# Kernel optimization log

Hardware: AMD Instinct MI355X
Metric: run time of the kernel (lower is better)

The kernel has to match this reference:

```python
import jax, jax.numpy as jnp
import numpy as np

B, S, D, H = 2, 2048, 1024, 16
DH = D // H


def setup_inputs() -> dict:
    key = jax.random.key(0)
    ks = jax.random.split(key, 13)
    s = 1.0 / np.sqrt(D)
    inp = {
        "q": jax.random.normal(ks[0], (B, S, D), jnp.float32),
        "k": jax.random.normal(ks[1], (B, S, D), jnp.float32),
        "v": jax.random.normal(ks[2], (B, S, D), jnp.float32),
        # causal mask [B,1,Q,K]: True = attend
        "attn_mask": jnp.broadcast_to(jnp.tril(jnp.ones((S, S), bool))[None, None], (B, 1, S, S)),
        "rel_bias": 0.1 * jax.random.normal(ks[3], (H, S, S), jnp.float32),
        "Wq": s * jax.random.normal(ks[4], (D, D), jnp.float32),
        "bq": jnp.zeros((D,), jnp.float32),
        "Wk": s * jax.random.normal(ks[5], (D, D), jnp.float32),
        "bk": jnp.zeros((D,), jnp.float32),
        "Wv": s * jax.random.normal(ks[6], (D, D), jnp.float32),
        "bv": jnp.zeros((D,), jnp.float32),
        "Wo": s * jax.random.normal(ks[7], (D, D), jnp.float32),
        "bo": jnp.zeros((D,), jnp.float32),
    }
    return inp


def reference(q, k, v, attn_mask, rel_bias, Wq, bq, Wk, bk, Wv, bv, Wo, bo):
    Bq, Q, Dm = q.shape
    K = k.shape[1]
    # projections -> [B, H, S, DH]
    qh = (q @ Wq + bq).reshape(Bq, Q, H, DH).transpose(0, 2, 1, 3)
    kh = (k @ Wk + bk).reshape(Bq, K, H, DH).transpose(0, 2, 1, 3)
    vh = (v @ Wv + bv).reshape(Bq, K, H, DH).transpose(0, 2, 1, 3)
    scores = jnp.einsum("bhqd,bhkd->bhqk", qh, kh) / np.sqrt(DH).astype(np.float32)
    scores = scores + rel_bias  # [H,Q,K] broadcasts over batch
    scores = jnp.where(attn_mask, scores, -jnp.inf)
    attn = jax.nn.softmax(scores, axis=-1)
    out = jnp.einsum("bhqk,bhkd->bhqd", attn, vh)
    out = out.transpose(0, 2, 1, 3).reshape(Bq, Q, Dm)
    return out @ Wo + bo
```

## Files before the change

### kernel.cpp

```cpp
#include <hip/hip_runtime.h>

typedef unsigned short u16;
typedef __attribute__((ext_vector_type(8))) short bf16x8;
typedef __attribute__((ext_vector_type(4))) float f32x4;
typedef __attribute__((ext_vector_type(4))) unsigned short us4;

#define B_ 2
#define S_ 2048
#define D_ 1024
#define H_ 16
#define DH_ 64
#define M_ 4096

__device__ __forceinline__ u16 f2bf(float f) {
  unsigned int u = __builtin_bit_cast(unsigned int, f);
  u += 0x7FFFu + ((u >> 16) & 1u);
  return (u16)(u >> 16);
}

__device__ __forceinline__ unsigned int cvtpk(float lo, float hi) {
  unsigned int r;
  asm("v_cvt_pk_bf16_f32 %0, %1, %2" : "=v"(r) : "v"(lo), "v"(hi));
  return r;
}

__device__ __forceinline__ float fexp2(float x) {
  float r;
  asm("v_exp_f32 %0, %1" : "=v"(r) : "v"(x));
  return r;
}

__device__ __forceinline__ void gload_lds16(const void* g, void* l) {
  __builtin_amdgcn_global_load_lds(
      (__attribute__((address_space(1))) void*)(g),
      (__attribute__((address_space(3))) void*)(l),
      16, 0, 0);
}

__global__ __launch_bounds__(256) void wprep_kernel(const float* __restrict__ W0,
                                                    const float* __restrict__ W1,
                                                    const float* __restrict__ W2,
                                                    const float* __restrict__ W3,
                                                    u16* __restrict__ Wt,
                                                    const float* __restrict__ qin,
                                                    const float* __restrict__ kin,
                                                    const float* __restrict__ vin,
                                                    u16* __restrict__ Xq,
                                                    u16* __restrict__ Xk,
                                                    u16* __restrict__ Xv) {
  int z = blockIdx.z;
  if (z < 4) {
    __shared__ float tile[32][33];
    const float* W = (z == 0) ? W0 : (z == 1) ? W1 : (z == 2) ? W2 : W3;
    u16* out = Wt + (size_t)z * D_ * D_;
    int tx = threadIdx.x, ty = threadIdx.y;
    int x = blockIdx.x * 32 + tx;
    for (int j = 0; j < 32; j += 8)
      tile[ty + j][tx] = W[(size_t)(blockIdx.y * 32 + ty + j) * D_ + x];
    __syncthreads();
    int x2 = blockIdx.y * 32 + tx;
    for (int j = 0; j < 32; j += 8)
      out[(size_t)(blockIdx.x * 32 + ty + j) * D_ + x2] = f2bf(tile[tx][ty + j]);
  } else {
    int zz = z - 4;
    const float* src = (zz == 0) ? qin : (zz == 1) ? kin : vin;
    u16* dst = (zz == 0) ? Xq : (zz == 1) ? Xk : Xv;
    int bid = blockIdx.y * 32 + blockIdx.x;
    int t = threadIdx.y * 32 + threadIdx.x;
    const float4* s4 = (const float4*)src;
    for (int i = 0; i < 4; ++i) {
      int idx = bid * 1024 + i * 256 + t;
      float4 v4 = s4[idx];
      us4 o;
      o[0] = f2bf(v4.x); o[1] = f2bf(v4.y); o[2] = f2bf(v4.z); o[3] = f2bf(v4.w);
      ((us4*)dst)[idx] = o;
    }
  }
}

__global__ __launch_bounds__(256) void gemm_qkv(const u16* __restrict__ Xq,
                                                const u16* __restrict__ Xk,
                                                const u16* __restrict__ Xv,
                                                const u16* __restrict__ Wt,
                                                const float* __restrict__ bq,
                                                const float* __restrict__ bk,
                                                const float* __restrict__ bv,
                                                u16* __restrict__ Qh,
                                                u16* __restrict__ Kh,
                                                u16* __restrict__ Vt) {
  __shared__ u16 As[128 * 32];
  __shared__ u16 Bs[128 * 32];
  int fid = blockIdx.x;
  int xcd = fid & 7, ii = fid >> 3;
  int grp = ii >> 3, yy = ii & 7;
  int gg = xcd * 12 + grp;
  int z = gg >> 5;
  int xx = gg & 31;
  const u16* A = (z == 0) ? Xq : (z == 1) ? Xk : Xv;
  const u16* Bt = Wt + (size_t)z * D_ * D_;
  const float* bias = (z == 0) ? bq : (z == 1) ? bk : bv;
  u16* O = (z == 0) ? Qh : (z == 1) ? Kh : Vt;

  int tid = threadIdx.x;
  int lane = tid & 63, wave = tid >> 6;
  int m0 = xx * 128, n0 = yy * 128;
  int wr = wave >> 1, wc = wave & 1;
  int fr = lane & 15, fk = (lane >> 4) * 8;

  f32x4 acc[4][4];
  const f32x4 vzero = {0.f, 0.f, 0.f, 0.f};
  for (int i = 0; i < 4; ++i)
    for (int j = 0; j < 4; ++j) acc[i][j] = vzero;

  for (int k0 = 0; k0 < D_; k0 += 32) {
    if (k0) __syncthreads();
    for (int i = 0; i < 2; ++i) {
      int wofs = ((i * 4 + wave) << 10);
      int ofs = wofs + lane * 16;
      int row = ofs >> 6;
      int cole = (ofs & 63) >> 1;
      gload_lds16(A + (size_t)(m0 + row) * D_ + k0 + cole, (char*)As + wofs);
      gload_lds16(Bt + (size_t)(n0 + row) * D_ + k0 + cole, (char*)Bs + wofs);
    }
    __syncthreads();
    bf16x8 af[4], bfr[4];
    for (int mi = 0; mi < 4; ++mi)
      af[mi] = *(const bf16x8*)(As + (wr * 64 + mi * 16 + fr) * 32 + fk);
    for (int ni = 0; ni < 4; ++ni)
      bfr[ni] = *(const bf16x8*)(Bs + (wc * 64 + ni * 16 + fr) * 32 + fk);
    for (int mi = 0; mi < 4; ++mi)
      for (int ni = 0; ni < 4; ++ni)
        acc[mi][ni] =
            __builtin_amdgcn_mfma_f32_16x16x32_bf16(af[mi], bfr[ni], acc[mi][ni], 0, 0, 0);
  }

  if (z == 2) {
    for (int mi = 0; mi < 4; ++mi) {
      int rowb = m0 + wr * 64 + mi * 16 + (lane >> 4) * 4;
      int bb2 = rowb >> 11, s0 = rowb & (S_ - 1);
      int l0 = s0 & 63;
      int p_local = ((l0 >> 5) & 1) * 32 + ((l0 >> 2) & 3) * 8 + ((l0 >> 4) & 1) * 4;
      int col2 = (s0 & ~63) | p_local;
      for (int ni = 0; ni < 4; ++ni) {
        int col = n0 + wc * 64 + ni * 16 + fr;
        int hh = col >> 6, dh = col & 63;
        float bv = bias[col];
        us4 pk;
        for (int r = 0; r < 4; ++r) pk[r] = f2bf(acc[mi][ni][r] + bv);
        *(us4*)(O + ((size_t)(bb2 * H_ + hh) * DH_ + dh) * S_ + col2) = pk;
      }
    }
  } else {
    float scale = (z == 0) ? 0.125f : 1.0f;
    for (int mi = 0; mi < 4; ++mi) {
      int rowb = m0 + wr * 64 + mi * 16 + (lane >> 4) * 4;
      for (int ni = 0; ni < 4; ++ni) {
        int col = n0 + wc * 64 + ni * 16 + fr;
        int hh = col >> 6, dh = col & 63;
        float bv = bias[col];
        for (int r = 0; r < 4; ++r) {
          int row = rowb + r;
          int bb2 = row >> 11, s = row & (S_ - 1);
          O[((size_t)(bb2 * H_ + hh) * S_ + s) * DH_ + dh] =
              f2bf((acc[mi][ni][r] + bv) * scale);
        }
      }
    }
  }
}

__global__ __launch_bounds__(256) void gemm_out(const u16* __restrict__ A,
                                                const u16* __restrict__ Bt,
                                                const float* __restrict__ bias,
                                                float* __restrict__ O) {
  __shared__ u16 As[64 * 32];
  __shared__ u16 Bs[128 * 32];
  int fid = blockIdx.x;
  int xcd = fid & 7, ii = fid >> 3;
  int grp = ii >> 3, yy = ii & 7;
  int gg = xcd * 8 + grp;
  int tid = threadIdx.x;
  int lane = tid & 63, wave = tid >> 6;
  int m0 = gg * 64, n0 = yy * 128;
  int fr = lane & 15, fk = (lane >> 4) * 8;

  f32x4 acc[4][2];
  const f32x4 vzero = {0.f, 0.f, 0.f, 0.f};
  for (int i = 0; i < 4; ++i)
    for (int j = 0; j < 2; ++j) acc[i][j] = vzero;

  for (int k0 = 0; k0 < D_; k0 += 32) {
    if (k0) __syncthreads();
    {
      int wofs = wave << 10;
      int ofs = wofs + lane * 16;
      int row = ofs >> 6;
      int cole = (ofs & 63) >> 1;
      gload_lds16(A + (size_t)(m0 + row) * D_ + k0 + cole, (char*)As + wofs);
    }
    for (int i = 0; i < 2; ++i) {
      int wofs = ((i * 4 + wave) << 10);
      int ofs = wofs + lane * 16;
      int row = ofs >> 6;
      int cole = (ofs & 63) >> 1;
      gload_lds16(Bt + (size_t)(n0 + row) * D_ + k0 + cole, (char*)Bs + wofs);
    }
    __syncthreads();
    bf16x8 af[4], bfr[2];
    for (int mi = 0; mi < 4; ++mi)
      af[mi] = *(const bf16x8*)(As + (mi * 16 + fr) * 32 + fk);
    for (int ni = 0; ni < 2; ++ni)
      bfr[ni] = *(const bf16x8*)(Bs + (wave * 32 + ni * 16 + fr) * 32 + fk);
    for (int mi = 0; mi < 4; ++mi)
      for (int ni = 0; ni < 2; ++ni)
        acc[mi][ni] =
            __builtin_amdgcn_mfma_f32_16x16x32_bf16(af[mi], bfr[ni], acc[mi][ni], 0, 0, 0);
  }

  for (int mi = 0; mi < 4; ++mi) {
    int rowb = m0 + mi * 16 + (lane >> 4) * 4;
    for (int ni = 0; ni < 2; ++ni) {
      int col = n0 + wave * 32 + ni * 16 + fr;
      float bv = bias[col];
      for (int r = 0; r < 4; ++r)
        O[(size_t)(rowb + r) * D_ + col] = acc[mi][ni][r] + bv;
    }
  }
}

__global__ __launch_bounds__(256, 4) void attn_kernel(const u16* __restrict__ Qh,
                                                      const u16* __restrict__ Kh,
                                                      const u16* __restrict__ Vt,
                                                      const float* __restrict__ relb,
                                                      u16* __restrict__ attnout) {
  __shared__ u16 KVs[2][2][4096];

  int fid = blockIdx.x;
  int rr = fid >> 8, c = fid & 255;
  int j = c >> 3, e = c & 7;
  int s = (rr & 1) ? j : 31 - j;
  int h = (rr & 1) ? e + 8 : e;
  int b = rr >> 1;

  int w = threadIdx.x >> 6, lane = threadIdx.x & 63;
  int fr = lane & 15, g = lane >> 4;
  int q0w = s * 64 + w * 16;
  int qme = q0w + fr;
  int bh = b * H_ + h;
  int sx = (fr & 7) << 4;

  int kind = w >> 1;
  int i0 = (w & 1) * 4;
  int srow_lo = lane >> 3;
  int scb = (lane & 7) * 16;

  const u16* Qb = Qh + ((size_t)bh * S_ + q0w) * DH_;
  bf16x8 qf0 = *(const bf16x8*)(Qb + fr * DH_ + 8 * g);
  bf16x8 qf1 = *(const bf16x8*)(Qb + fr * DH_ + 32 + 8 * g);

  const float* Bq = relb + (size_t)h * S_ * S_ + (size_t)qme * S_ + 4 * g;
  const float LOG2E = 1.44269504f;

  int T = s + 1;

  auto STAGE = [&](int buf, int kb) {
    for (int i = 0; i < 4; ++i) {
      int ii = i0 + i;
      int row = ii * 8 + srow_lo;
      int cbs = scb ^ ((row & 7) << 4);
      const u16* src;
      if (kind == 0)
        src = Kh + ((size_t)bh * S_ + kb + row) * DH_ + (cbs >> 1);
      else
        src = Vt + ((size_t)bh * DH_ + row) * S_ + kb + (cbs >> 1);
      gload_lds16(src, &KVs[kind][buf][ii * 512]);
    }
  };

  f32x4 acc[4];
  const f32x4 vzero = {0.f, 0.f, 0.f, 0.f};
  for (int f4 = 0; f4 < 4; ++f4) acc[f4] = vzero;
  float m = -1.0e4f, l = 0.f;

  STAGE(0, 0);
  f32x4 bi[4], bn[4];
  for (int cc = 0; cc < 4; ++cc) bi[cc] = *(const f32x4*)(Bq + 16 * cc);
  __syncthreads();

  for (int t = 0; t < T; ++t) {
    int kb = t * 64;
    int buf = t & 1;
    bool diag = (t == T - 1);
    if (!diag) {
      STAGE(buf ^ 1, kb + 64);
      for (int cc = 0; cc < 4; ++cc) bn[cc] = *(const f32x4*)(Bq + kb + 64 + 16 * cc);
    }

    const u16* Kt = &KVs[0][buf][0];
    const u16* Vl = &KVs[1][buf][0];

    f32x4 sc[4];
    __builtin_amdgcn_s_setprio(1);
    for (int cc = 0; cc < 4; ++cc) {
      bf16x8 k0 = *(const bf16x8*)(Kt + (16 * cc + fr) * 64 + (((16 * g) ^ sx) >> 1));
      bf16x8 k1 = *(const bf16x8*)(Kt + (16 * cc + fr) * 64 + (((64 + 16 * g) ^ sx) >> 1));
      f32x4 z = __builtin_amdgcn_mfma_f32_16x16x32_bf16(k0, qf0, bi[cc], 0, 0, 0);
      z = __builtin_amdgcn_mfma_f32_16x16x32_bf16(k1, qf1, z, 0, 0, 0);
      sc[cc] = z;
    }
    __builtin_amdgcn_s_setprio(0);
    if (diag) {
      for (int cc = 0; cc < 4; ++cc)
        for (int r = 0; r < 4; ++r) {
          int key = kb + 16 * cc + 4 * g + r;
          sc[cc][r] = (key <= qme) ? sc[cc][r] : -1e30f;
        }
    }
    float pm = sc[0][0];
    for (int cc = 0; cc < 4; ++cc)
      for (int r = 0; r < 4; ++r) pm = fmaxf(pm, sc[cc][r]);
    pm = fmaxf(pm, __shfl_xor(pm, 16));
    pm = fmaxf(pm, __shfl_xor(pm, 32));
    if (!__all(pm - m <= 8.0f)) {
      float mn = fmaxf(m, pm);
      float corr = __expf(m - mn);
      m = mn;
      l *= corr;
      float c0 = __shfl(corr, 4 * g + 0);
      float c1 = __shfl(corr, 4 * g + 1);
      float c2 = __shfl(corr, 4 * g + 2);
      float c3 = __shfl(corr, 4 * g + 3);
      for (int f4 = 0; f4 < 4; ++f4) {
        acc[f4][0] *= c0; acc[f4][1] *= c1; acc[f4][2] *= c2; acc[f4][3] *= c3;
      }
    }
    float nms = m * -LOG2E;
    float rs = 0.f;
    for (int cc = 0; cc < 4; ++cc)
      for (int r = 0; r < 4; ++r) {
        sc[cc][r] = fexp2(fmaf(sc[cc][r], LOG2E, nms));
        rs += sc[cc][r];
      }
    l += rs;
    union { unsigned int w4[4]; bf16x8 v; } pp[2];
    for (int jj = 0; jj < 2; ++jj) {
      pp[jj].w4[0] = cvtpk(sc[2 * jj][0], sc[2 * jj][1]);
      pp[jj].w4[1] = cvtpk(sc[2 * jj][2], sc[2 * jj][3]);
      pp[jj].w4[2] = cvtpk(sc[2 * jj + 1][0], sc[2 * jj + 1][1]);
      pp[jj].w4[3] = cvtpk(sc[2 * jj + 1][2], sc[2 * jj + 1][3]);
    }
    __builtin_amdgcn_s_setprio(1);
    for (int f4 = 0; f4 < 4; ++f4) {
      for (int jj = 0; jj < 2; ++jj) {
        bf16x8 vv = *(const bf16x8*)(Vl + (f4 * 16 + fr) * 64 +
                                     (((jj * 64 + g * 16) ^ sx) >> 1));
        acc[f4] = __builtin_amdgcn_mfma_f32_16x16x32_bf16(pp[jj].v, vv, acc[f4], 0, 0, 0);
      }
    }
    __builtin_amdgcn_s_setprio(0);
    for (int cc = 0; cc < 4; ++cc) bi[cc] = bn[cc];
    __syncthreads();
  }

  l += __shfl_xor(l, 16);
  l += __shfl_xor(l, 32);
  float il = 1.f / l;
  for (int r = 0; r < 4; ++r) {
    float ilr = __shfl(il, 4 * g + r);
    int qq = q0w + 4 * g + r;
    u16* ob = attnout + ((size_t)b * S_ + qq) * D_ + h * 64;
    for (int f4 = 0; f4 < 4; ++f4) ob[f4 * 16 + fr] = f2bf(acc[f4][r] * ilr);
  }
}

extern "C" void kernel_launch(void* const* d_in, const int* in_sizes, int n_in,
                              void* d_out, int out_size, void* d_ws, size_t ws_size,
                              hipStream_t stream) {
  const float* q = (const float*)d_in[0];
  const float* k = (const float*)d_in[1];
  const float* v = (const float*)d_in[2];
  const float* rb = (const float*)d_in[4];
  const float* Wq = (const float*)d_in[5];
  const float* bq = (const float*)d_in[6];
  const float* Wk = (const float*)d_in[7];
  const float* bk = (const float*)d_in[8];
  const float* Wv = (const float*)d_in[9];
  const float* bv = (const float*)d_in[10];
  const float* Wo = (const float*)d_in[11];
  const float* bo = (const float*)d_in[12];
  float* out = (float*)d_out;

  char* ws = (char*)d_ws;
  const size_t SZ = (size_t)M_ * D_ * 2;
  u16* Xq = (u16*)(ws);
  u16* Xk = (u16*)(ws + SZ);
  u16* Xv = (u16*)(ws + 2 * SZ);
  u16* Qh = (u16*)(ws + 3 * SZ);
  u16* Kh = (u16*)(ws + 4 * SZ);
  u16* Vt = (u16*)(ws + 5 * SZ);
  u16* Wt = (u16*)(ws + 6 * SZ);
  u16* Xb = Xq;

  wprep_kernel<<<dim3(32, 32, 7), dim3(32, 8), 0, stream>>>(Wq, Wk, Wv, Wo, Wt,
                                                            q, k, v, Xq, Xk, Xv);

  gemm_qkv<<<dim3(768), 256, 0, stream>>>(Xq, Xk, Xv, Wt, bq, bk, bv, Qh, Kh, Vt);

  attn_kernel<<<dim3(1024), 256, 0, stream>>>(Qh, Kh, Vt, rb, Xb);

  gemm_out<<<dim3(512), 256, 0, stream>>>(Xb, Wt + 3 * (size_t)D_ * D_, bo, out);
}
```

Baseline: 140.3 us.

## Fuse fp32-to-bf16 activation conversion into QKV GEMM A-tile loads

The separate pass that turned q/k/v from fp32 into bf16 workspace buffers is removed. The QKV GEMM now loads fp32 A tiles directly into LDS with an XOR swizzle and converts them to bf16 with packed cvt instructions just before the MFMAs. This avoids writing and re-reading about 24 MB of intermediate bf16 activations. In exchange, each k-step loads twice the A bytes from global memory, uses twice the LDS for A, and adds conversion ALU work inside the inner loop.

Result: slower. 157.4 us (+12.2%).

```diff
diff --git a/kernel.cpp b/kernel.cpp
--- a/kernel.cpp
+++ b/kernel.cpp
@@ -41,46 +41,24 @@
                                                     const float* __restrict__ W1,
                                                     const float* __restrict__ W2,
                                                     const float* __restrict__ W3,
-                                                    u16* __restrict__ Wt,
-                                                    const float* __restrict__ qin,
-                                                    const float* __restrict__ kin,
-                                                    const float* __restrict__ vin,
-                                                    u16* __restrict__ Xq,
-                                                    u16* __restrict__ Xk,
-                                                    u16* __restrict__ Xv) {
+                                                    u16* __restrict__ Wt) {
+  __shared__ float tile[32][33];
   int z = blockIdx.z;
-  if (z < 4) {
-    __shared__ float tile[32][33];
-    const float* W = (z == 0) ? W0 : (z == 1) ? W1 : (z == 2) ? W2 : W3;
-    u16* out = Wt + (size_t)z * D_ * D_;
-    int tx = threadIdx.x, ty = threadIdx.y;
-    int x = blockIdx.x * 32 + tx;
-    for (int j = 0; j < 32; j += 8)
-      tile[ty + j][tx] = W[(size_t)(blockIdx.y * 32 + ty + j) * D_ + x];
-    __syncthreads();
-    int x2 = blockIdx.y * 32 + tx;
-    for (int j = 0; j < 32; j += 8)
-      out[(size_t)(blockIdx.x * 32 + ty + j) * D_ + x2] = f2bf(tile[tx][ty + j]);
-  } else {
-    int zz = z - 4;
-    const float* src = (zz == 0) ? qin : (zz == 1) ? kin : vin;
-    u16* dst = (zz == 0) ? Xq : (zz == 1) ? Xk : Xv;
-    int bid = blockIdx.y * 32 + blockIdx.x;
-    int t = threadIdx.y * 32 + threadIdx.x;
-    const float4* s4 = (const float4*)src;
-    for (int i = 0; i < 4; ++i) {
-      int idx = bid * 1024 + i * 256 + t;
-      float4 v4 = s4[idx];
-      us4 o;
-      o[0] = f2bf(v4.x); o[1] = f2bf(v4.y); o[2] = f2bf(v4.z); o[3] = f2bf(v4.w);
-      ((us4*)dst)[idx] = o;
-    }
-  }
-}
-
-__global__ __launch_bounds__(256) void gemm_qkv(const u16* __restrict__ Xq,
-                                                const u16* __restrict__ Xk,
-                                                const u16* __restrict__ Xv,
+  const float* W = (z == 0) ? W0 : (z == 1) ? W1 : (z == 2) ? W2 : W3;
+  u16* out = Wt + (size_t)z * D_ * D_;
+  int tx = threadIdx.x, ty = threadIdx.y;
+  int x = blockIdx.x * 32 + tx;
+  for (int j = 0; j < 32; j += 8)
+    tile[ty + j][tx] = W[(size_t)(blockIdx.y * 32 + ty + j) * D_ + x];
+  __syncthreads();
+  int x2 = blockIdx.y * 32 + tx;
+  for (int j = 0; j < 32; j += 8)
+    out[(size_t)(blockIdx.x * 32 + ty + j) * D_ + x2] = f2bf(tile[tx][ty + j]);
+}
+
+__global__ __launch_bounds__(256) void gemm_qkv(const float* __restrict__ qin,
+                                                const float* __restrict__ kin,
+                                                const float* __restrict__ vin,
                                                 const u16* __restrict__ Wt,
                                                 const float* __restrict__ bq,
                                                 const float* __restrict__ bk,
@@ -88,7 +66,7 @@
                                                 u16* __restrict__ Qh,
                                                 u16* __restrict__ Kh,
                                                 u16* __restrict__ Vt) {
-  __shared__ u16 As[128 * 32];
+  __shared__ __align__(16) char AsfB[128 * 32 * 4];
   __shared__ u16 Bs[128 * 32];
   int fid = blockIdx.x;
   int xcd = fid & 7, ii = fid >> 3;
@@ -96,7 +74,7 @@
   int gg = xcd * 12 + grp;
   int z = gg >> 5;
   int xx = gg & 31;
-  const u16* A = (z == 0) ? Xq : (z == 1) ? Xk : Xv;
+  const float* A = (z == 0) ? qin : (z == 1) ? kin : vin;
   const u16* Bt = Wt + (size_t)z * D_ * D_;
   const float* bias = (z == 0) ? bq : (z == 1) ? bk : bv;
   u16* O = (z == 0) ? Qh : (z == 1) ? Kh : Vt;
@@ -114,18 +92,36 @@
 
   for (int k0 = 0; k0 < D_; k0 += 32) {
     if (k0) __syncthreads();
+    for (int i = 0; i < 4; ++i) {
+      int lin = ((i * 4 + wave) << 10) + lane * 16;
+      int row = lin >> 7;
+      int colb = lin & 127;
+      int scolb = colb ^ ((row & 7) << 4);
+      gload_lds16(A + (size_t)(m0 + row) * D_ + k0 + (scolb >> 2),
+                  AsfB + ((i * 4 + wave) << 10));
+    }
     for (int i = 0; i < 2; ++i) {
       int wofs = ((i * 4 + wave) << 10);
       int ofs = wofs + lane * 16;
       int row = ofs >> 6;
       int cole = (ofs & 63) >> 1;
-      gload_lds16(A + (size_t)(m0 + row) * D_ + k0 + cole, (char*)As + wofs);
       gload_lds16(Bt + (size_t)(n0 + row) * D_ + k0 + cole, (char*)Bs + wofs);
     }
     __syncthreads();
     bf16x8 af[4], bfr[4];
-    for (int mi = 0; mi < 4; ++mi)
-      af[mi] = *(const bf16x8*)(As + (wr * 64 + mi * 16 + fr) * 32 + fk);
+    for (int mi = 0; mi < 4; ++mi) {
+      int row = wr * 64 + mi * 16 + fr;
+      const char* base = AsfB + row * 128;
+      int swz = (row & 7) << 4;
+      f32x4 a0 = *(const f32x4*)(base + ((fk * 4) ^ swz));
+      f32x4 a1 = *(const f32x4*)(base + ((fk * 4 + 16) ^ swz));
+      union { unsigned int w4[4]; bf16x8 v; } af_;
+      af_.w4[0] = cvtpk(a0[0], a0[1]);
+      af_.w4[1] = cvtpk(a0[2], a0[3]);
+      af_.w4[2] = cvtpk(a1[0], a1[1]);
+      af_.w4[3] = cvtpk(a1[2], a1[3]);
+      af[mi] = af_.v;
+    }
     for (int ni = 0; ni < 4; ++ni)
       bfr[ni] = *(const bf16x8*)(Bs + (wc * 64 + ni * 16 + fr) * 32 + fk);
     for (int mi = 0; mi < 4; ++mi)
@@ -392,19 +388,15 @@
 
   char* ws = (char*)d_ws;
   const size_t SZ = (size_t)M_ * D_ * 2;
-  u16* Xq = (u16*)(ws);
-  u16* Xk = (u16*)(ws + SZ);
-  u16* Xv = (u16*)(ws + 2 * SZ);
-  u16* Qh = (u16*)(ws + 3 * SZ);
-  u16* Kh = (u16*)(ws + 4 * SZ);
-  u16* Vt = (u16*)(ws + 5 * SZ);
-  u16* Wt = (u16*)(ws + 6 * SZ);
-  u16* Xb = Xq;
-
-  wprep_kernel<<<dim3(32, 32, 7), dim3(32, 8), 0, stream>>>(Wq, Wk, Wv, Wo, Wt,
-                                                            q, k, v, Xq, Xk, Xv);
-
-  gemm_qkv<<<dim3(768), 256, 0, stream>>>(Xq, Xk, Xv, Wt, bq, bk, bv, Qh, Kh, Vt);
+  u16* Xb = (u16*)(ws);
+  u16* Qh = (u16*)(ws + SZ);
+  u16* Kh = (u16*)(ws + 2 * SZ);
+  u16* Vt = (u16*)(ws + 3 * SZ);
+  u16* Wt = (u16*)(ws + 4 * SZ);
+
+  wprep_kernel<<<dim3(32, 32, 4), dim3(32, 8), 0, stream>>>(Wq, Wk, Wv, Wo, Wt);
+
+  gemm_qkv<<<dim3(768), 256, 0, stream>>>(q, k, v, Wt, bq, bk, bv, Qh, Kh, Vt);
 
   attn_kernel<<<dim3(1024), 256, 0, stream>>>(Qh, Kh, Vt, rb, Xb);
 
```
